# Performance work log

Measured on AMD Instinct MI355X. Metric: run time of the kernel, lower is better.

The kernel has to match this reference:

```python
import jax, jax.numpy as jnp
import numpy as np

B, C, CB, WIDTH = 16, 256, 64, 32
F = CB * WIDTH  # lstm_features = 2048


def setup_inputs() -> dict:
    key = jax.random.key(0)
    ks = jax.random.split(key, 14)
    s = 0.02  # ~1/sqrt(F), torch default uniform(-1/sqrt(h), 1/sqrt(h)) scale
    return {
        "x": jax.random.normal(ks[0], (B, C, WIDTH, WIDTH), jnp.float32),
        "w_in": jax.random.normal(ks[1], (CB, C), jnp.float32) * s,
        "b_in": jax.random.normal(ks[2], (CB,), jnp.float32) * s,
        "W_ih0": jax.random.normal(ks[3], (4 * F, F), jnp.float32) * s,
        "W_hh0": jax.random.normal(ks[4], (4 * F, F), jnp.float32) * s,
        "b_ih0": jax.random.normal(ks[5], (4 * F,), jnp.float32) * s,
        "b_hh0": jax.random.normal(ks[6], (4 * F,), jnp.float32) * s,
        "W_ih1": jax.random.normal(ks[7], (4 * F, F), jnp.float32) * s,
        "W_hh1": jax.random.normal(ks[8], (4 * F, F), jnp.float32) * s,
        "b_ih1": jax.random.normal(ks[9], (4 * F,), jnp.float32) * s,
        "b_hh1": jax.random.normal(ks[10], (4 * F,), jnp.float32) * s,
        "w_out": jax.random.normal(ks[11], (C, CB), jnp.float32) * s,
        "b_out": jax.random.normal(ks[12], (C,), jnp.float32) * s,
    }


def _lstm_cell(x_t, h, c, W_ih, W_hh, b_ih, b_hh):
    # torch nn.LSTM gate order: i, f, g, o
    g = x_t @ W_ih.T + h @ W_hh.T + (b_ih + b_hh)
    i, f, gg, o = jnp.split(g, 4, axis=-1)
    c_n = jax.nn.sigmoid(f) * c + jax.nn.sigmoid(i) * jnp.tanh(gg)
    h_n = jax.nn.sigmoid(o) * jnp.tanh(c_n)
    return h_n, c_n


def reference(x, w_in, b_in, W_ih0, W_hh0, b_ih0, b_hh0,
              W_ih1, W_hh1, b_ih1, b_hh1, w_out, b_out):
    Bn, Cn, H, W = x.shape
    # 1x1 conv bottleneck in -> [B, Cb, H, W]
    bn = jnp.einsum('bchw,oc->bohw', x, w_in) + b_in[None, :, None, None]
    Cb = bn.shape[1]
    Ff = W * Cb
    # rows as sequence: [H, B, W*Cb], feature index = w*Cb + c
    seq = bn.transpose(2, 0, 3, 1).reshape(H, Bn, Ff)

    def step(states, x_t):
        h0, c0, h1, c1 = states
        h0, c0 = _lstm_cell(x_t, h0, c0, W_ih0, W_hh0, b_ih0, b_hh0)
        h1, c1 = _lstm_cell(h0, h1, c1, W_ih1, W_hh1, b_ih1, b_hh1)
        return (h0, c0, h1, c1), h1

    z = jnp.zeros((Bn, Ff), x.dtype)
    states, outs = jax.lax.scan(step, (z, z, z, z), seq)
    y0 = outs[-1]  # out[-1]: first generated row

    def gen(carry, _):
        st, y = carry
        st, y_n = step(st, y)
        return (st, y_n), y_n

    _, gen_outs = jax.lax.scan(gen, (states, y0), None, length=W - 1)
    seq_out = jnp.concatenate([y0[None], gen_outs], axis=0)  # [W, B, F]

    # un-flatten back to spatial: [B, S=W, W, Cb] then 1x1 conv out -> [B, C, S, W]
    spatial = seq_out.transpose(1, 0, 2).reshape(Bn, W, W, Cb)
    y = jnp.einsum('bswc,oc->bosw', spatial, w_out) + b_out[None, :, None, None]
    # stitch generated rows below input along height dim
    return jnp.concatenate([x, y], axis=2)
```

## Files before the change

kernel.cpp:

```cpp
#include <hip/hip_runtime.h>
#include <hip/hip_bf16.h>

typedef unsigned short u16;
typedef unsigned char uchar;
typedef unsigned long long u64;
typedef float f32x4 __attribute__((ext_vector_type(4)));
typedef int i8v __attribute__((ext_vector_type(8)));

#define FDIM 2048
#define NBLK 256
#define NSTEP 63
#define SLOT 32768

__device__ __forceinline__ u16 f2b(float x) {
    __hip_bfloat16 h = __float2bfloat16(x);
    return __builtin_bit_cast(u16, h);
}
__device__ __forceinline__ float b2f(u16 u) {
    __hip_bfloat16 h = __builtin_bit_cast(__hip_bfloat16, u);
    return __bfloat162float(h);
}
__device__ __forceinline__ float sigm(float x) { return 1.0f / (1.0f + __expf(-x)); }
__device__ __forceinline__ float tanh_f(float x) { return 1.0f - 2.0f / (__expf(2.0f * x) + 1.0f); }

__device__ __forceinline__ unsigned f2fp8(float x) {
    unsigned u = __builtin_bit_cast(unsigned, x);
    unsigned s = (u >> 24) & 0x80u;
    unsigned mag = u & 0x7fffffffu;
    if (mag >= 0x43E80000u) return s | 0x7Eu;
    int e = (int)(mag >> 23) - 127;
    if (e >= -6) {
        unsigned m = mag + 0x7FFFFu + ((mag >> 20) & 1u);
        unsigned e8 = (m >> 23) - 127 + 7;
        unsigned m3 = (m >> 20) & 7u;
        if (e8 >= 16u) return s | 0x7Eu;
        return s | (e8 << 3) | m3;
    }
    float ax = __builtin_bit_cast(float, mag);
    int d = (int)__builtin_rintf(ax * 512.0f);
    return s | (unsigned)d;
}

__device__ __forceinline__ unsigned q_e2m1(float v) {
    unsigned s = (v < 0.f) ? 8u : 0u;
    float a = fabsf(v);
    unsigned q;
    if (a < 0.25f) q = 0;
    else if (a < 0.75f) q = 1;
    else if (a < 1.25f) q = 2;
    else if (a < 1.75f) q = 3;
    else if (a < 2.5f)  q = 4;
    else if (a < 3.5f)  q = 5;
    else if (a < 5.0f)  q = 6;
    else q = 7;
    return s | q;
}

__global__ __launch_bounds__(256) void k_pack4(const float* __restrict__ W0, const float* __restrict__ W1,
                                               const float* __restrict__ W2, const float* __restrict__ W3,
                                               uchar* __restrict__ Wp4, uchar* __restrict__ scl) {
    __shared__ float lw[64][132];
    int idx = blockIdx.x;
    int kt = idx & 15, m = (idx >> 4) & 1, gb = idx >> 5;
    int fam = gb >> 7, blf = gb & 127;
    const float* src = (fam == 0) ? (m == 0 ? W0 : W1) : (m == 0 ? W2 : W3);
    int tid = threadIdx.x;
    for (int i = tid; i < 64 * 32; i += 256) {
        int r = i >> 5, c4 = i & 31;
        const float* p = src + (size_t)((r >> 4) * 2048 + blf * 16 + (r & 15)) * 2048 + kt * 128 + c4 * 4;
        float4 v = *(const float4*)p;
        lw[r][c4 * 4 + 0] = v.x; lw[r][c4 * 4 + 1] = v.y;
        lw[r][c4 * 4 + 2] = v.z; lw[r][c4 * 4 + 3] = v.w;
    }
    __syncthreads();
    {
        int jt = tid >> 6, l = tid & 63;
        int r = jt * 16 + (l & 15);
        int k0 = (l >> 4) * 32;
        float mx = 0.f;
#pragma unroll
        for (int e = 0; e < 32; ++e) mx = fmaxf(mx, fabsf(lw[r][k0 + e]));
        int ee = -127;
        if (mx > 0.f) {
            ee = (int)ceilf(log2f(mx * (1.0f / 6.0f)));
            if (ee < -127) ee = -127;
            if (ee > 127) ee = 127;
        }
        float inv = exp2f((float)(-ee));
        unsigned wd[4];
#pragma unroll
        for (int d = 0; d < 4; ++d) {
            unsigned acc = 0;
#pragma unroll
            for (int bi = 0; bi < 4; ++bi) {
                float v0 = lw[r][k0 + d * 8 + 2 * bi] * inv;
                float v1 = lw[r][k0 + d * 8 + 2 * bi + 1] * inv;
                acc |= (q_e2m1(v0) << (bi * 8)) | (q_e2m1(v1) << (bi * 8 + 4));
            }
            wd[d] = acc;
        }
        size_t wo = (size_t)gb * 131072 + (size_t)((m * 4 + jt) * 16 + kt) * 1024 + (size_t)l * 16;
        *(uint4*)(Wp4 + wo) = make_uint4(wd[0], wd[1], wd[2], wd[3]);
        scl[(size_t)gb * 8192 + (size_t)((m * 4 + jt) * 64 + l) * 16 + kt] = (uchar)(ee + 127);
    }
}

__global__ void k_bias(const float* __restrict__ bi0, const float* __restrict__ bh0,
                       const float* __restrict__ bi1, const float* __restrict__ bh1,
                       float* __restrict__ bias0, float* __restrict__ bias1) {
    int i = blockIdx.x * blockDim.x + threadIdx.x;
    if (i < 4 * FDIM) {
        bias0[i] = bi0[i] + bh0[i];
        bias1[i] = bi1[i] + bh1[i];
    }
}

__global__ __launch_bounds__(256) void k_seqprep(const float* __restrict__ x,
                                                 const float* __restrict__ w_in,
                                                 const float* __restrict__ b_in,
                                                 uchar* __restrict__ seqb) {
    int h = blockIdx.x >> 4, b = blockIdx.x & 15;
    __shared__ float xs[256][32];
    __shared__ float wl[64][257];
    int tid = threadIdx.x;
    for (int i = tid; i < 256 * 32; i += 256) {
        int c = i >> 5, w = i & 31;
        xs[c][w] = x[(((size_t)b * 256 + c) * 32 + h) * 32 + w];
    }
    for (int i = tid; i < 64 * 256; i += 256) {
        int cb = i >> 8, c = i & 255;
        wl[cb][c] = w_in[i];
    }
    __syncthreads();
    int w = (tid * 8) >> 6, cb0 = (tid * 8) & 63;
    float acc[8];
#pragma unroll
    for (int j = 0; j < 8; ++j) acc[j] = b_in[cb0 + j];
    for (int c = 0; c < 256; ++c) {
        float xv = xs[c][w];
#pragma unroll
        for (int j = 0; j < 8; ++j) acc[j] += xv * wl[cb0 + j][c];
    }
    unsigned lo = 0, hi2 = 0;
#pragma unroll
    for (int j = 0; j < 4; ++j) lo |= f2fp8(acc[j] * 4.0f) << (j * 8);
#pragma unroll
    for (int j = 0; j < 4; ++j) hi2 |= f2fp8(acc[4 + j] * 4.0f) << (j * 8);
    int kt = tid >> 4, kq = (tid >> 2) & 3, e0 = (tid & 3) * 8;
    uchar* dst = seqb + (size_t)h * SLOT + (size_t)kt * 2048 + (size_t)(b + 16 * kq) * 32 + e0;
    *(uint2*)dst = make_uint2(lo, hi2);
}

__global__ __launch_bounds__(576, 1) void k_lstm(const uchar* __restrict__ Wp4,
                                                 const uchar* __restrict__ scl,
                                                 const float* __restrict__ bias0,
                                                 const float* __restrict__ bias1,
                                                 const uchar* __restrict__ seqb,
                                                 uchar* __restrict__ H0, uchar* __restrict__ H1,
                                                 u16* __restrict__ seqout,
                                                 unsigned* __restrict__ tags0,
                                                 unsigned* __restrict__ tags1) {
    __shared__ uchar wlds[131072];
    __shared__ float gbuf[4][4][16][16];
    __shared__ u64 hs_st[16][2];
    __shared__ unsigned flag0LDS, flag1LDS, w6done;
    const int tid = threadIdx.x, lane = tid & 63, w = tid >> 6;
    const int jp = w & 1, kh = (w >> 1) & 1, m = w >> 2;
    const int bl = blockIdx.x;
    const int fam = bl >> 7, blf = bl & 127;

    {
        const uchar* src = Wp4 + (size_t)bl * 131072;
        for (int i = tid; i < 8192; i += 576)
            *(uint4*)(wlds + (size_t)i * 16) = *(const uint4*)(src + (size_t)i * 16);
    }
    unsigned sw00 = 0, sw01 = 0, sw10 = 0, sw11 = 0;
    if (w < 8) {
        const uchar* sbase = scl + (size_t)bl * 8192 + (size_t)((m * 4 + jp * 2) * 64 + lane) * 16;
        uint4 s0 = *(const uint4*)(sbase);
        uint4 s1 = *(const uint4*)(sbase + 1024);
        sw00 = kh ? s0.z : s0.x; sw01 = kh ? s0.w : s0.y;
        sw10 = kh ? s1.z : s1.x; sw11 = kh ? s1.w : s1.y;
    }
    float bw[2][4];
    float cs[2] = {0.f, 0.f};
    const int wvoff = (w == 7) ? 8 : 0;
    if (w >= 6) {
        const int flb = (lane & 3) * 2;
        const float* barr = fam ? bias1 : bias0;
#pragma unroll
        for (int i = 0; i < 2; ++i) {
            int col = blf * 16 + wvoff + flb + i;
#pragma unroll
            for (int g = 0; g < 4; ++g) bw[i][g] = barr[g * FDIM + col];
        }
    }
    if (tid == 0) { flag0LDS = 0; flag1LDS = 0; w6done = 0; }
    __syncthreads();

    unsigned f0 = 0, f1 = 0;
    const int b16 = lane & 15, kq = lane >> 4;

    for (int s = 0; s < NSTEP; ++s) {
        if (w == 8) {
            int t0 = fam ? (s + 1) : s;
            int t1 = fam ? s : ((s >= 32) ? s : 0);
#define ADV(F, TGT, TB, FL)                                                            \
            while ((int)F < (TGT)) {                                                   \
                const unsigned* trow = (TB) + (size_t)F * 4096;                        \
                const unsigned* t0p = trow + (size_t)lane * 32;                        \
                const unsigned* t1p = trow + (size_t)(lane + 64) * 32;                 \
                while (__hip_atomic_load(t0p, __ATOMIC_RELAXED,                        \
                                         __HIP_MEMORY_SCOPE_AGENT) != 1u)              \
                    __builtin_amdgcn_s_sleep(4);                                       \
                while (__hip_atomic_load(t1p, __ATOMIC_RELAXED,                        \
                                         __HIP_MEMORY_SCOPE_AGENT) != 1u)              \
                    __builtin_amdgcn_s_sleep(4);                                       \
                ++F;                                                                   \
                if (lane == 0)                                                         \
                    __hip_atomic_store(&(FL), F, __ATOMIC_RELAXED,                     \
                                       __HIP_MEMORY_SCOPE_WORKGROUP);                  \
            }
            if (fam == 0) { ADV(f0, t0, tags0, flag0LDS) ADV(f1, t1, tags1, flag1LDS) }
            else          { ADV(f1, t1, tags1, flag1LDS) ADV(f0, t0, tags0, flag0LDS) }
#undef ADV
        } else {
            unsigned need0 = 0, need1 = 0;
            if (fam == 0) { if (m) need0 = (unsigned)s; else need1 = (s >= 32) ? (unsigned)s : 0u; }
            else          { if (m) need1 = (unsigned)s; else need0 = (unsigned)(s + 1); }
            if (need0)
                while (__hip_atomic_load(&flag0LDS, __ATOMIC_RELAXED,
                                         __HIP_MEMORY_SCOPE_WORKGROUP) < need0)
                    __builtin_amdgcn_s_sleep(1);
            if (need1)
                while (__hip_atomic_load(&flag1LDS, __ATOMIC_RELAXED,
                                         __HIP_MEMORY_SCOPE_WORKGROUP) < need1)
                    __builtin_amdgcn_s_sleep(1);
            asm volatile("" ::: "memory");

            const uchar* xsrc = fam ? (H0 + (size_t)(s + 1) * SLOT)
                              : (s < 32 ? seqb + (size_t)s * SLOT : H1 + (size_t)s * SLOT);
            const uchar* hsrc = fam ? (H1 + (size_t)s * SLOT) : (H0 + (size_t)s * SLOT);
            const uchar* asrc = m ? hsrc : xsrc;

            const uchar* ap = asrc + (size_t)lane * 32;
            uint4 A[8][2];
#pragma unroll
            for (int t = 0; t < 8; ++t) {
                A[t][0] = *(const uint4*)(ap + (size_t)(kh * 8 + t) * 2048);
                A[t][1] = *(const uint4*)(ap + (size_t)(kh * 8 + t) * 2048 + 16);
            }
            const uchar* bp0 = wlds + (size_t)((m * 4 + jp * 2) * 16 + kh * 8) * 1024 + lane * 16;
            const uchar* bp1 = bp0 + 16384;

            f32x4 aA0 = {0.f,0.f,0.f,0.f}, aA1 = {0.f,0.f,0.f,0.f};
            f32x4 aB0 = {0.f,0.f,0.f,0.f}, aB1 = {0.f,0.f,0.f,0.f};
#define MF(T)                                                                          \
            {                                                                          \
                uint4 alo = A[T][0], ahi = A[T][1];                                    \
                i8v av = {(int)alo.x, (int)alo.y, (int)alo.z, (int)alo.w,              \
                          (int)ahi.x, (int)ahi.y, (int)ahi.z, (int)ahi.w};             \
                uint4 b0 = *(const uint4*)(bp0 + (T) * 1024);                          \
                i8v bv0 = {(int)b0.x, (int)b0.y, (int)b0.z, (int)b0.w, 0, 0, 0, 0};    \
                uint4 b1 = *(const uint4*)(bp1 + (T) * 1024);                          \
                i8v bv1 = {(int)b1.x, (int)b1.y, (int)b1.z, (int)b1.w, 0, 0, 0, 0};    \
                if ((T) & 1) {                                                         \
                    aA1 = __builtin_amdgcn_mfma_scale_f32_16x16x128_f8f6f4(            \
                        av, bv0, aA1, 0, 4, 0, 127, (T) & 3,                           \
                        (int)((T) < 4 ? sw00 : sw01));                                 \
                    aB1 = __builtin_amdgcn_mfma_scale_f32_16x16x128_f8f6f4(            \
                        av, bv1, aB1, 0, 4, 0, 127, (T) & 3,                           \
                        (int)((T) < 4 ? sw10 : sw11));                                 \
                } else {                                                               \
                    aA0 = __builtin_amdgcn_mfma_scale_f32_16x16x128_f8f6f4(            \
                        av, bv0, aA0, 0, 4, 0, 127, (T) & 3,                           \
                        (int)((T) < 4 ? sw00 : sw01));                                 \
                    aB0 = __builtin_amdgcn_mfma_scale_f32_16x16x128_f8f6f4(            \
                        av, bv1, aB0, 0, 4, 0, 127, (T) & 3,                           \
                        (int)((T) < 4 ? sw10 : sw11));                                 \
                }                                                                      \
            }
            MF(0) MF(1) MF(2) MF(3) MF(4) MF(5) MF(6) MF(7)
#undef MF
            f32x4 rA = aA0 + aA1, rB = aB0 + aB1;
            const int slot = m * 2 + kh;
#pragma unroll
            for (int i = 0; i < 4; ++i) {
                gbuf[jp * 2 + 0][slot][kq * 4 + i][b16] = rA[i];
                gbuf[jp * 2 + 1][slot][kq * 4 + i][b16] = rB[i];
            }
        }
        __syncthreads();

        float gsum[2][4];
        if (w >= 6) {
            const int b = lane >> 2, flb = (lane & 3) * 2;
#pragma unroll
            for (int i = 0; i < 2; ++i) {
                const int f = wvoff + flb + i;
#pragma unroll
                for (int g = 0; g < 4; ++g)
                    gsum[i][g] = gbuf[g][0][b][f] + gbuf[g][1][b][f]
                               + gbuf[g][2][b][f] + gbuf[g][3][b][f];
            }
        }
        __syncthreads();

        if (w >= 6) {
            const int b = lane >> 2, flb = (lane & 3) * 2;
            u16 hb2 = 0;
            float hnv[2];
#pragma unroll
            for (int i = 0; i < 2; ++i) {
                float gv[4];
#pragma unroll
                for (int g = 0; g < 4; ++g) gv[g] = gsum[i][g] * 0.25f + bw[i][g];
                float cn = sigm(gv[1]) * cs[i] + sigm(gv[0]) * tanh_f(gv[2]);
                float hn = sigm(gv[3]) * tanh_f(cn);
                cs[i] = cn;
                hb2 |= (u16)(f2fp8(hn * 4.0f) << (8 * i));
                hnv[i] = hn;
            }
            const int wv = wvoff >> 3;
            *(u16*)((uchar*)&hs_st[b][wv] + flb) = hb2;
            asm volatile("s_waitcnt lgkmcnt(0)" ::: "memory");
            uchar* out = (fam ? H1 : H0) + (size_t)(s + 1) * SLOT;
            if (lane < 16) {
                const int kt0 = blf >> 3, sub = (blf & 7) >> 1, byte0 = (blf & 1) * 16;
                size_t o = (size_t)kt0 * 2048 + (size_t)(lane + 16 * sub) * 32 + byte0 + wvoff;
                __hip_atomic_store((u64*)(out + o), hs_st[lane][wv],
                                   __ATOMIC_RELAXED, __HIP_MEMORY_SCOPE_AGENT);
            }
            asm volatile("s_waitcnt vmcnt(0)" ::: "memory");
            if (w == 6) {
                if (lane == 0)
                    __hip_atomic_store(&w6done, (unsigned)(s + 1),
                                       __ATOMIC_RELAXED, __HIP_MEMORY_SCOPE_WORKGROUP);
            } else {
                if (lane == 0) {
                    while (__hip_atomic_load(&w6done, __ATOMIC_RELAXED,
                                             __HIP_MEMORY_SCOPE_WORKGROUP) < (unsigned)(s + 1))
                        ;
                    unsigned* tg = (fam ? tags1 : tags0) + (size_t)s * 4096 + (size_t)blf * 32;
                    __hip_atomic_store(tg, 1u, __ATOMIC_RELAXED, __HIP_MEMORY_SCOPE_AGENT);
                }
            }
            if (fam && s >= 31) {
                unsigned pk = (unsigned)f2b(hnv[0]) | ((unsigned)f2b(hnv[1]) << 16);
                *(unsigned*)(seqout + (size_t)(s - 31) * 16 * FDIM
                             + (size_t)b * FDIM + blf * 16 + wvoff + flb) = pk;
            }
        }
    }
}

__global__ void k_copyx(const float* __restrict__ x, float* __restrict__ out) {
    size_t n = (size_t)4096 * 256;
    size_t stride = (size_t)gridDim.x * blockDim.x;
    for (size_t i = (size_t)blockIdx.x * blockDim.x + threadIdx.x; i < n; i += stride) {
        size_t bc = i >> 8, r = i & 255;
        ((float4*)out)[bc * 512 + r] = ((const float4*)x)[i];
    }
}

__global__ __launch_bounds__(256) void k_convout(const u16* __restrict__ seqout,
                                                 const float* __restrict__ w_out,
                                                 const float* __restrict__ b_out,
                                                 float* __restrict__ out) {
    int s = blockIdx.x >> 4, b = blockIdx.x & 15;
    __shared__ float srow[2048];
    int tid = threadIdx.x;
    for (int i = tid; i < 2048; i += 256) srow[i] = b2f(seqout[((size_t)s * 16 + b) * FDIM + i]);
    __syncthreads();
    int o = tid;
    float bo = b_out[o];
    float wreg[64];
#pragma unroll
    for (int cb = 0; cb < 64; ++cb) wreg[cb] = w_out[o * 64 + cb];
    for (int w4 = 0; w4 < 8; ++w4) {
        float ac0 = bo, ac1 = bo, ac2 = bo, ac3 = bo;
#pragma unroll
        for (int cb = 0; cb < 64; ++cb) {
            float wv = wreg[cb];
            ac0 += srow[(w4 * 4 + 0) * 64 + cb] * wv;
            ac1 += srow[(w4 * 4 + 1) * 64 + cb] * wv;
            ac2 += srow[(w4 * 4 + 2) * 64 + cb] * wv;
            ac3 += srow[(w4 * 4 + 3) * 64 + cb] * wv;
        }
        float4 v; v.x = ac0; v.y = ac1; v.z = ac2; v.w = ac3;
        *(float4*)&out[(((size_t)b * 256 + o) * 64 + 32 + s) * 32 + w4 * 4] = v;
    }
}

extern "C" void kernel_launch(void* const* d_in, const int* in_sizes, int n_in,
                              void* d_out, int out_size, void* d_ws, size_t ws_size,
                              hipStream_t stream) {
    const float* x    = (const float*)d_in[0];
    const float* w_in = (const float*)d_in[1];
    const float* b_in = (const float*)d_in[2];
    const float* Wih0 = (const float*)d_in[3];
    const float* Whh0 = (const float*)d_in[4];
    const float* bih0 = (const float*)d_in[5];
    const float* bhh0 = (const float*)d_in[6];
    const float* Wih1 = (const float*)d_in[7];
    const float* Whh1 = (const float*)d_in[8];
    const float* bih1 = (const float*)d_in[9];
    const float* bhh1 = (const float*)d_in[10];
    const float* wout = (const float*)d_in[11];
    const float* bout = (const float*)d_in[12];
    float* out = (float*)d_out;
    char* ws = (char*)d_ws;
    const size_t BF = (size_t)16 * FDIM;

    uchar* Wp4 = (uchar*)ws;
    size_t off = (size_t)NBLK * 131072;
    uchar* scl = (uchar*)(ws + off); off += (size_t)NBLK * 8192;
    float* bias0 = (float*)(ws + off); off += 4 * FDIM * 4;
    float* bias1 = (float*)(ws + off); off += 4 * FDIM * 4;
    uchar* seqb = (uchar*)(ws + off); off += (size_t)32 * SLOT;
    u16* seqout = (u16*)(ws + off); off += (size_t)32 * BF * 2;
    uchar* H0 = (uchar*)(ws + off); off += (size_t)64 * SLOT;
    uchar* H1 = (uchar*)(ws + off); off += (size_t)64 * SLOT;
    off = (off + 127) & ~(size_t)127;
    unsigned* tags0 = (unsigned*)(ws + off); size_t tagoff = off;
    off += (size_t)NSTEP * 4096 * 4;
    unsigned* tags1 = (unsigned*)(ws + off);
    off += (size_t)NSTEP * 4096 * 4;

    hipMemsetAsync(H0, 0, SLOT, stream);
    hipMemsetAsync(H1, 0, SLOT, stream);
    hipMemsetAsync(ws + tagoff, 0, off - tagoff, stream);

    k_pack4<<<8192, 256, 0, stream>>>(Wih0, Whh0, Wih1, Whh1, Wp4, scl);
    k_bias<<<32, 256, 0, stream>>>(bih0, bhh0, bih1, bhh1, bias0, bias1);
    k_seqprep<<<512, 256, 0, stream>>>(x, w_in, b_in, seqb);
    k_lstm<<<NBLK, 576, 0, stream>>>(Wp4, scl, bias0, bias1, seqb, H0, H1, seqout, tags0, tags1);
    k_copyx<<<2048, 256, 0, stream>>>(x, out);
    k_convout<<<512, 256, 0, stream>>>(seqout, wout, bout, out);
}
```

Before: 603.7 us.

## Fuse weight quantization, bias sum and x copy into the persistent LSTM kernel

The separate FP4 weight-packing and bias-summing kernels are folded into the LSTM kernel's prologue. Each block now quantizes its own weight slice straight into LDS, and the scales go to LDS instead of global memory. The copy of x into the output is moved into the LSTM kernel, where two waves do it while spin-waiting on step flags. This removes several launches and the global round trip of packed weights, at the cost of a heavier per-block prologue (strided fp32 reads plus quantization by 576 threads) and possible interference with the latency-critical recurrent loop.

```diff
diff --git a/kernel.cpp b/kernel.cpp
--- a/kernel.cpp
+++ b/kernel.cpp
@@ -56,65 +56,6 @@
     return s | q;
 }
 
-__global__ __launch_bounds__(256) void k_pack4(const float* __restrict__ W0, const float* __restrict__ W1,
-                                               const float* __restrict__ W2, const float* __restrict__ W3,
-                                               uchar* __restrict__ Wp4, uchar* __restrict__ scl) {
-    __shared__ float lw[64][132];
-    int idx = blockIdx.x;
-    int kt = idx & 15, m = (idx >> 4) & 1, gb = idx >> 5;
-    int fam = gb >> 7, blf = gb & 127;
-    const float* src = (fam == 0) ? (m == 0 ? W0 : W1) : (m == 0 ? W2 : W3);
-    int tid = threadIdx.x;
-    for (int i = tid; i < 64 * 32; i += 256) {
-        int r = i >> 5, c4 = i & 31;
-        const float* p = src + (size_t)((r >> 4) * 2048 + blf * 16 + (r & 15)) * 2048 + kt * 128 + c4 * 4;
-        float4 v = *(const float4*)p;
-        lw[r][c4 * 4 + 0] = v.x; lw[r][c4 * 4 + 1] = v.y;
-        lw[r][c4 * 4 + 2] = v.z; lw[r][c4 * 4 + 3] = v.w;
-    }
-    __syncthreads();
-    {
-        int jt = tid >> 6, l = tid & 63;
-        int r = jt * 16 + (l & 15);
-        int k0 = (l >> 4) * 32;
-        float mx = 0.f;
-#pragma unroll
-        for (int e = 0; e < 32; ++e) mx = fmaxf(mx, fabsf(lw[r][k0 + e]));
-        int ee = -127;
-        if (mx > 0.f) {
-            ee = (int)ceilf(log2f(mx * (1.0f / 6.0f)));
-            if (ee < -127) ee = -127;
-            if (ee > 127) ee = 127;
-        }
-        float inv = exp2f((float)(-ee));
-        unsigned wd[4];
-#pragma unroll
-        for (int d = 0; d < 4; ++d) {
-            unsigned acc = 0;
-#pragma unroll
-            for (int bi = 0; bi < 4; ++bi) {
-                float v0 = lw[r][k0 + d * 8 + 2 * bi] * inv;
-                float v1 = lw[r][k0 + d * 8 + 2 * bi + 1] * inv;
-                acc |= (q_e2m1(v0) << (bi * 8)) | (q_e2m1(v1) << (bi * 8 + 4));
-            }
-            wd[d] = acc;
-        }
-        size_t wo = (size_t)gb * 131072 + (size_t)((m * 4 + jt) * 16 + kt) * 1024 + (size_t)l * 16;
-        *(uint4*)(Wp4 + wo) = make_uint4(wd[0], wd[1], wd[2], wd[3]);
-        scl[(size_t)gb * 8192 + (size_t)((m * 4 + jt) * 64 + l) * 16 + kt] = (uchar)(ee + 127);
-    }
-}
-
-__global__ void k_bias(const float* __restrict__ bi0, const float* __restrict__ bh0,
-                       const float* __restrict__ bi1, const float* __restrict__ bh1,
-                       float* __restrict__ bias0, float* __restrict__ bias1) {
-    int i = blockIdx.x * blockDim.x + threadIdx.x;
-    if (i < 4 * FDIM) {
-        bias0[i] = bi0[i] + bh0[i];
-        bias1[i] = bi1[i] + bh1[i];
-    }
-}
-
 __global__ __launch_bounds__(256) void k_seqprep(const float* __restrict__ x,
                                                  const float* __restrict__ w_in,
                                                  const float* __restrict__ b_in,
@@ -151,16 +92,23 @@
     *(uint2*)dst = make_uint2(lo, hi2);
 }
 
-__global__ __launch_bounds__(576, 1) void k_lstm(const uchar* __restrict__ Wp4,
-                                                 const uchar* __restrict__ scl,
-                                                 const float* __restrict__ bias0,
-                                                 const float* __restrict__ bias1,
+__global__ __launch_bounds__(576, 1) void k_lstm(const float* __restrict__ Wih0,
+                                                 const float* __restrict__ Whh0,
+                                                 const float* __restrict__ Wih1,
+                                                 const float* __restrict__ Whh1,
+                                                 const float* __restrict__ bih0,
+                                                 const float* __restrict__ bhh0,
+                                                 const float* __restrict__ bih1,
+                                                 const float* __restrict__ bhh1,
                                                  const uchar* __restrict__ seqb,
                                                  uchar* __restrict__ H0, uchar* __restrict__ H1,
                                                  u16* __restrict__ seqout,
                                                  unsigned* __restrict__ tags0,
-                                                 unsigned* __restrict__ tags1) {
+                                                 unsigned* __restrict__ tags1,
+                                                 const float* __restrict__ xg,
+                                                 float* __restrict__ outg) {
     __shared__ uchar wlds[131072];
+    __shared__ uchar sclLDS[8192];
     __shared__ float gbuf[4][4][16][16];
     __shared__ u64 hs_st[16][2];
     __shared__ unsigned flag0LDS, flag1LDS, w6done;
@@ -170,13 +118,52 @@
     const int fam = bl >> 7, blf = bl & 127;
 
     {
-        const uchar* src = Wp4 + (size_t)bl * 131072;
-        for (int i = tid; i < 8192; i += 576)
-            *(uint4*)(wlds + (size_t)i * 16) = *(const uint4*)(src + (size_t)i * 16);
-    }
+        const float* srcA = fam ? Wih1 : Wih0;
+        const float* srcB = fam ? Whh1 : Whh0;
+        for (int e = tid; e < 8192; e += 576) {
+            int l = e & 63, kt = (e >> 6) & 15, jt = (e >> 10) & 3, mm = e >> 12;
+            const float* src = mm ? srcB : srcA;
+            const float* p = src + (size_t)(jt * 2048 + blf * 16 + (l & 15)) * 2048
+                           + kt * 128 + (l >> 4) * 32;
+            float v[32];
+#pragma unroll
+            for (int j = 0; j < 8; ++j) {
+                float4 q = *(const float4*)(p + j * 4);
+                v[j * 4 + 0] = q.x; v[j * 4 + 1] = q.y;
+                v[j * 4 + 2] = q.z; v[j * 4 + 3] = q.w;
+            }
+            float mx = 0.f;
+#pragma unroll
+            for (int ei = 0; ei < 32; ++ei) mx = fmaxf(mx, fabsf(v[ei]));
+            int ee = -127;
+            if (mx > 0.f) {
+                ee = (int)ceilf(log2f(mx * (1.0f / 6.0f)));
+                if (ee < -127) ee = -127;
+                if (ee > 127) ee = 127;
+            }
+            float inv = exp2f((float)(-ee));
+            unsigned wd[4];
+#pragma unroll
+            for (int d = 0; d < 4; ++d) {
+                unsigned acc = 0;
+#pragma unroll
+                for (int bi = 0; bi < 4; ++bi) {
+                    float v0 = v[d * 8 + 2 * bi] * inv;
+                    float v1 = v[d * 8 + 2 * bi + 1] * inv;
+                    acc |= (q_e2m1(v0) << (bi * 8)) | (q_e2m1(v1) << (bi * 8 + 4));
+                }
+                wd[d] = acc;
+            }
+            *(uint4*)(wlds + (size_t)e * 16) = make_uint4(wd[0], wd[1], wd[2], wd[3]);
+            sclLDS[(size_t)((mm * 4 + jt) * 64 + l) * 16 + kt] = (uchar)(ee + 127);
+        }
+    }
+    if (tid == 0) { flag0LDS = 0; flag1LDS = 0; w6done = 0; }
+    __syncthreads();
+
     unsigned sw00 = 0, sw01 = 0, sw10 = 0, sw11 = 0;
     if (w < 8) {
-        const uchar* sbase = scl + (size_t)bl * 8192 + (size_t)((m * 4 + jp * 2) * 64 + lane) * 16;
+        const uchar* sbase = sclLDS + (size_t)((m * 4 + jp * 2) * 64 + lane) * 16;
         uint4 s0 = *(const uint4*)(sbase);
         uint4 s1 = *(const uint4*)(sbase + 1024);
         sw00 = kh ? s0.z : s0.x; sw01 = kh ? s0.w : s0.y;
@@ -187,16 +174,27 @@
     const int wvoff = (w == 7) ? 8 : 0;
     if (w >= 6) {
         const int flb = (lane & 3) * 2;
-        const float* barr = fam ? bias1 : bias0;
+        const float* bi_ = fam ? bih1 : bih0;
+        const float* bh_ = fam ? bhh1 : bhh0;
 #pragma unroll
         for (int i = 0; i < 2; ++i) {
             int col = blf * 16 + wvoff + flb + i;
 #pragma unroll
-            for (int g = 0; g < 4; ++g) bw[i][g] = barr[g * FDIM + col];
-        }
-    }
-    if (tid == 0) { flag0LDS = 0; flag1LDS = 0; w6done = 0; }
-    __syncthreads();
+            for (int g = 0; g < 4; ++g)
+                bw[i][g] = bi_[g * FDIM + col] + bh_[g * FDIM + col];
+        }
+    }
+    const bool steal = (w == 4) || (w == 5);
+    int myC = (w == 5) ? 32 : 0;
+    const int endC = steal ? ((w == 5) ? 64 : 32) : 0;
+#define CPY1()                                                                         \
+    {                                                                                  \
+        size_t ii = (size_t)bl * 4096 + (size_t)myC * 64 + lane;                       \
+        float4 vv = ((const float4*)xg)[ii];                                           \
+        ((float4*)outg)[(ii >> 8) * 512 + (ii & 255)] = vv;                            \
+        asm volatile("s_waitcnt vmcnt(0)" ::: "memory");                               \
+        ++myC;                                                                         \
+    }
 
     unsigned f0 = 0, f1 = 0;
     const int b16 = lane & 15, kq = lane >> 4;
@@ -228,14 +226,18 @@
             unsigned need0 = 0, need1 = 0;
             if (fam == 0) { if (m) need0 = (unsigned)s; else need1 = (s >= 32) ? (unsigned)s : 0u; }
             else          { if (m) need1 = (unsigned)s; else need0 = (unsigned)(s + 1); }
-            if (need0)
+            if (need0) {
                 while (__hip_atomic_load(&flag0LDS, __ATOMIC_RELAXED,
-                                         __HIP_MEMORY_SCOPE_WORKGROUP) < need0)
-                    __builtin_amdgcn_s_sleep(1);
-            if (need1)
+                                         __HIP_MEMORY_SCOPE_WORKGROUP) < need0) {
+                    if (steal && myC < endC) { CPY1() } else __builtin_amdgcn_s_sleep(1);
+                }
+            }
+            if (need1) {
                 while (__hip_atomic_load(&flag1LDS, __ATOMIC_RELAXED,
-                                         __HIP_MEMORY_SCOPE_WORKGROUP) < need1)
-                    __builtin_amdgcn_s_sleep(1);
+                                         __HIP_MEMORY_SCOPE_WORKGROUP) < need1) {
+                    if (steal && myC < endC) { CPY1() } else __builtin_amdgcn_s_sleep(1);
+                }
+            }
             asm volatile("" ::: "memory");
 
             const uchar* xsrc = fam ? (H0 + (size_t)(s + 1) * SLOT)
@@ -352,15 +354,8 @@
             }
         }
     }
-}
-
-__global__ void k_copyx(const float* __restrict__ x, float* __restrict__ out) {
-    size_t n = (size_t)4096 * 256;
-    size_t stride = (size_t)gridDim.x * blockDim.x;
-    for (size_t i = (size_t)blockIdx.x * blockDim.x + threadIdx.x; i < n; i += stride) {
-        size_t bc = i >> 8, r = i & 255;
-        ((float4*)out)[bc * 512 + r] = ((const float4*)x)[i];
-    }
+    if (steal) while (myC < endC) CPY1()
+#undef CPY1
 }
 
 __global__ __launch_bounds__(256) void k_convout(const u16* __restrict__ seqout,
@@ -412,11 +407,7 @@
     char* ws = (char*)d_ws;
     const size_t BF = (size_t)16 * FDIM;
 
-    uchar* Wp4 = (uchar*)ws;
-    size_t off = (size_t)NBLK * 131072;
-    uchar* scl = (uchar*)(ws + off); off += (size_t)NBLK * 8192;
-    float* bias0 = (float*)(ws + off); off += 4 * FDIM * 4;
-    float* bias1 = (float*)(ws + off); off += 4 * FDIM * 4;
+    size_t off = 0;
     uchar* seqb = (uchar*)(ws + off); off += (size_t)32 * SLOT;
     u16* seqout = (u16*)(ws + off); off += (size_t)32 * BF * 2;
     uchar* H0 = (uchar*)(ws + off); off += (size_t)64 * SLOT;
@@ -431,10 +422,9 @@
     hipMemsetAsync(H1, 0, SLOT, stream);
     hipMemsetAsync(ws + tagoff, 0, off - tagoff, stream);
 
-    k_pack4<<<8192, 256, 0, stream>>>(Wih0, Whh0, Wih1, Whh1, Wp4, scl);
-    k_bias<<<32, 256, 0, stream>>>(bih0, bhh0, bih1, bhh1, bias0, bias1);
     k_seqprep<<<512, 256, 0, stream>>>(x, w_in, b_in, seqb);
-    k_lstm<<<NBLK, 576, 0, stream>>>(Wp4, scl, bias0, bias1, seqb, H0, H1, seqout, tags0, tags1);
-    k_copyx<<<2048, 256, 0, stream>>>(x, out);
+    k_lstm<<<NBLK, 576, 0, stream>>>(Wih0, Whh0, Wih1, Whh1,
+                                     bih0, bhh0, bih1, bhh1,
+                                     seqb, H0, H1, seqout, tags0, tags1, x, out);
     k_convout<<<512, 256, 0, stream>>>(seqout, wout, bout, out);
 }
```

Result: faster. 584.1 us (-3.2%).
